# Kernel tuning notes

Measured on AMD Instinct MI355X. Metric: run time of the kernel, lower is better.

## Reference

```python
import jax, jax.numpy as jnp
import numpy as np

OUT_CH = 19  # out_channels


def setup_inputs() -> dict:
    key = jax.random.key(0)
    ks = jax.random.split(key, 8)
    N1, N2, C = 8000, 8000, 96
    return {
        "sur_sv_feature": jax.random.normal(ks[0], (N2, C), jnp.float32),
        "sur_sv_coords": jax.random.uniform(ks[1], (N2, 3), jnp.float32, -20.0, 20.0),
        "sur_sv_gt": jax.random.randint(ks[2], (N2,), 0, OUT_CH, dtype=jnp.int32),
        "sv_prob": jax.random.normal(ks[3], (N1, OUT_CH), jnp.float32),
        "mean_features": jax.random.normal(ks[4], (N1, C), jnp.float32),
        "ori_coords": jax.random.uniform(ks[5], (N1, 3), jnp.float32, -20.0, 20.0),
        # well-conditioned invertible 4x4 homogeneous poses
        "posses": jnp.eye(4, dtype=jnp.float32)[None, :, :] + 0.05 * jax.random.normal(ks[6], (2, 4, 4), jnp.float32),
        "sv_gt_idx": jax.random.randint(ks[7], (N2,), 0, N1, dtype=jnp.int32),  # unused in forward
        "lg": 8000,
    }


def _alignment(coords, posses):
    # rev=1 branch: diff = inv(poses[1]) @ poses[0]; aligned = (diff @ [coords,1]^T)^T[:, :3]
    diff = jnp.linalg.inv(posses[1]) @ posses[0]
    homo = jnp.concatenate([coords, jnp.ones((coords.shape[0], 1), coords.dtype)], axis=1)
    return (homo @ diff.T)[:, :3]


def reference(sur_sv_feature, sur_sv_coords, sur_sv_gt, sv_prob, mean_features, ori_coords, posses, sv_gt_idx, lg):
    N1 = sv_prob.shape[0]
    al = _alignment(sur_sv_coords, posses)  # [N2,3]
    # cosine distance [N1,N2]
    w1 = jnp.linalg.norm(mean_features, axis=1, keepdims=True)
    w2 = jnp.linalg.norm(sur_sv_feature, axis=1, keepdims=True)
    feat_dist_cos = 1.0 - (mean_features @ sur_sv_feature.T) / jnp.maximum(w1 * w2.T, 1e-8)
    # squared L2 distance [N1,N2], scaled by 1/0.5^2
    xn = jnp.sum(ori_coords ** 2, axis=1)[:, None]
    yn = jnp.sum(al ** 2, axis=1)[None, :]
    coords_dist = jnp.maximum(xn + yn - 2.0 * (ori_coords @ al.T), 0.0) / 0.25
    support = (coords_dist < 100.0).astype(jnp.float32)  # 10**2 radius gate
    onehot = jnp.eye(OUT_CH, dtype=jnp.float32)[sur_sv_gt]  # [N2,19]
    dist_matric = 1.0 + feat_dist_cos - jnp.exp(-0.5 * coords_dist)
    K = jnp.exp(-dist_matric / 0.03) * support
    # 'Sinkhorn' loop: b,a depend only on constants u1,u2, so each of the 10
    # iterations computes identical values -> compute once (bit-identical).
    u2 = jnp.full((K.shape[0],), 1.0 / K.shape[0], jnp.float32)
    u1 = jnp.full((K.shape[1],), 1.0 / K.shape[1], jnp.float32)
    b = u2 / (K @ u1 + 1e-16)      # [N1]
    a = u1 / (K.T @ u2 + 1e-16)    # [N2]
    # diag(a) @ K.T @ diag(b) = a[:,None] * K.T * b[None,:]  -> [N2,N1]
    sim = (a[:, None] * K.T) * b[None, :]
    sim = sim[:lg]
    sv_prob_updated = jax.nn.softmax(sv_prob, axis=1)
    sm_index = jnp.argmax(sim, axis=1)          # [lg] indices into N1
    tmpx = sur_sv_gt[:lg]                       # onehot[:lg].argmax == gt labels
    vals = sv_prob_updated[sm_index, tmpx]      # diag(P[sm_index].index_select(1,tmpx))
    mask = jnp.where(jnp.any(vals > 0.1), vals > 0.1, vals > 0.0)
    scatter_idx = jnp.where(mask, sm_index, N1)  # out-of-bounds sentinel -> dropped
    sv_prob_new = sv_prob_updated.at[scatter_idx].set(onehot[:lg], mode='drop')
    # torch.unique(sm_index[tmp]); padded with -1 for jit-static shape
    trust = jnp.unique(jnp.where(mask, sm_index, -1), size=lg, fill_value=-1)
    pre = jnp.argmax(sv_prob_new, axis=1)
    return (trust, mean_features, ori_coords, pre, sv_prob_new, trust)
```

## Files before the change

kernel.cpp:

```cpp
#include <hip/hip_runtime.h>

#define N 8000
#define C 96
#define C4 24
#define OCH 19
#define NCELL 1000
#define NCH 32
#define HSZ (NCH*NCELL)
#define U1 (1.0f/8000.0f)
#define PAIR_CAP 256

__device__ __forceinline__ int clamp10(int v) { return min(max(v, 0), 9); }

__global__ void __launch_bounds__(256) k_prep(
    const float* __restrict__ sf, const float* __restrict__ coords,
    const float* __restrict__ posses,
    float* __restrict__ w2, float4* __restrict__ alN,
    int* __restrict__ cellB, int* __restrict__ histB,
    int4* __restrict__ ck4, int4* __restrict__ wn4, int* __restrict__ flags) {
    int bx = blockIdx.x, tid = threadIdx.x;
    if (bx < 32) {
        __shared__ int lhist[NCELL];
        __shared__ float sdiff[12];
        for (int c = tid; c < NCELL; c += 256) lhist[c] = 0;
        int j = bx*256 + tid;
        if (tid == 0) {
            double M[4][8];
            for (int r = 0; r < 4; ++r)
                for (int c = 0; c < 4; ++c) {
                    M[r][c] = (double)posses[16 + r*4 + c];
                    M[r][4+c] = (r == c) ? 1.0 : 0.0;
                }
            for (int col = 0; col < 4; ++col) {
                int piv = col; double best = fabs(M[col][col]);
                for (int r = col+1; r < 4; ++r) { double v = fabs(M[r][col]); if (v > best) { best = v; piv = r; } }
                if (piv != col) for (int c = 0; c < 8; ++c) { double t = M[col][c]; M[col][c] = M[piv][c]; M[piv][c] = t; }
                double inv = 1.0 / M[col][col];
                for (int c = 0; c < 8; ++c) M[col][c] *= inv;
                for (int r = 0; r < 4; ++r) if (r != col) {
                    double f = M[r][col];
                    for (int c = 0; c < 8; ++c) M[r][c] -= f * M[col][c];
                }
            }
            for (int r = 0; r < 3; ++r)
                for (int c = 0; c < 4; ++c) {
                    double sm = 0.0;
                    for (int k = 0; k < 4; ++k) sm += M[r][4+k] * (double)posses[k*4 + c];
                    sdiff[r*4 + c] = (float)sm;
                }
        }
        __syncthreads();
        if (j < N) {
            float c0 = coords[j*3], c1 = coords[j*3+1], c2 = coords[j*3+2];
            float a0 = (sdiff[0]*c0 + sdiff[1]*c1) + (sdiff[2]*c2 + sdiff[3]);
            float a1 = (sdiff[4]*c0 + sdiff[5]*c1) + (sdiff[6]*c2 + sdiff[7]);
            float a2 = (sdiff[8]*c0 + sdiff[9]*c1) + (sdiff[10]*c2 + sdiff[11]);
            alN[j] = make_float4(a0, a1, a2, a0*a0 + a1*a1 + a2*a2);
            int cx = clamp10((int)floorf((a0 + 25.f) * 0.2f));
            int cy = clamp10((int)floorf((a1 + 25.f) * 0.2f));
            int cz = clamp10((int)floorf((a2 + 25.f) * 0.2f));
            int cc = (cz*10 + cy)*10 + cx;
            cellB[j] = cc;
            atomicAdd(&lhist[cc], 1);
        }
        __syncthreads();
        for (int c = tid; c < NCELL; c += 256) histB[bx*NCELL + c] = lhist[c];
    } else if (bx < 64) {
        int b = bx - 32;
        int u = tid & 3;
        #pragma unroll
        for (int p0 = 0; p0 < 256; p0 += 64) {
            int jp = b*256 + p0 + (tid >> 2);
            float ax = 0.f, ay = 0.f, az = 0.f, aw = 0.f;
            if (jp < N) {
                const float4* s4 = (const float4*)sf + jp*C4;
                #pragma unroll
                for (int s2 = 0; s2 < 6; ++s2) {
                    float4 v = s4[s2*4 + u];
                    ax += v.x*v.x; ay += v.y*v.y; az += v.z*v.z; aw += v.w*v.w;
                }
            }
            float pp = (ax + ay) + (az + aw);
            pp += __shfl_xor(pp, 1);
            pp += __shfl_xor(pp, 2);
            if (jp < N && u == 0) w2[jp] = sqrtf(pp);
        }
    } else {
        int t0 = (bx-64)*256 + tid;
        int4 z = make_int4(0, 0, 0, 0);
        int4 f = make_int4(-1, -1, -1, -1);
        for (int t = t0; t < 8000; t += 16*256) {
            if (t < 4000) ck4[t] = z;
            else wn4[t-4000] = f;
        }
        if (bx == 64 && tid < 8) flags[tid] = 0;
    }
}

__global__ void __launch_bounds__(1024) k_scan(int* __restrict__ h, int* __restrict__ cs) {
    int t = threadIdx.x;
    int v[NCH]; int tot = 0;
    if (t < NCELL) {
        #pragma unroll
        for (int ch = 0; ch < NCH; ++ch) { int x = h[ch*NCELL + t]; v[ch] = x; tot += x; }
    }
    int x = tot;
    int lane = t & 63, wv = t >> 6;
    for (int off = 1; off < 64; off <<= 1) { int y = __shfl_up(x, off); if (lane >= off) x += y; }
    __shared__ int wtot[16];
    if (lane == 63) wtot[wv] = x;
    __syncthreads();
    int wpre = 0;
    for (int k = 0; k < 16; ++k) if (k < wv) wpre += wtot[k];
    int base = wpre + x - tot;
    if (t < NCELL) {
        cs[t] = base;
        int run = base;
        #pragma unroll
        for (int ch = 0; ch < NCH; ++ch) { h[ch*NCELL + t] = run; run += v[ch]; }
    }
    if (t == 0) cs[NCELL] = N;
}

__global__ void k_scatter(const int* __restrict__ cellB, const int* __restrict__ startT,
                          const float* __restrict__ w2, const float4* __restrict__ alN,
                          int* __restrict__ idBR, float* __restrict__ w2R, float4* __restrict__ alR) {
    __shared__ int sc[256];
    int chunk = blockIdx.x, tid = threadIdx.x;
    int gi = chunk*256 + tid;
    int cell = (gi < N) ? cellB[gi] : -1;
    sc[tid] = cell;
    __syncthreads();
    if (gi >= N) return;
    int rank = 0;
    const int4* sc4 = (const int4*)sc;
    int full = tid >> 2;
    for (int t4 = 0; t4 < full; ++t4) {
        int4 q = sc4[t4];
        rank += (q.x == cell) + (q.y == cell) + (q.z == cell) + (q.w == cell);
    }
    for (int t = full*4; t < tid; ++t) rank += (sc[t] == cell);
    int pos = startT[chunk*NCELL + cell] + rank;
    idBR[pos] = gi;
    w2R[pos] = w2[gi];
    alR[pos] = alN[gi];
}

__global__ void __launch_bounds__(256) k_pairs(
    const float4* __restrict__ mf4, const float* __restrict__ ori,
    const float4* __restrict__ alR, const float* __restrict__ w2R,
    const float4* __restrict__ sf4, const int* __restrict__ idBR,
    const int* __restrict__ csB,
    unsigned long long* __restrict__ colkey) {
    __shared__ float4 sRow[4][C4];
    __shared__ int bgi[4][128];
    __shared__ float bc[4][128];
    __shared__ float bw[4][128];
    __shared__ int sJ[4][PAIR_CAP];
    __shared__ float sK[4][PAIR_CAP];

    int tid = threadIdx.x, lane = tid & 63, w = tid >> 6;
    int i = blockIdx.x * 4 + w;
    if (lane < C4) sRow[w][lane] = mf4[i*C4 + lane];
    __syncthreads();

    float ox = ori[i*3], oy = ori[i*3+1], oz = ori[i*3+2];
    float xnv = ox*ox + oy*oy + oz*oz;
    float s = 0.f;
    for (int kk = 0; kk < C4; ++kk) {
        float4 v = sRow[w][kk];
        s += v.x*v.x; s += v.y*v.y; s += v.z*v.z; s += v.w*v.w;
    }
    float w1v = sqrtf(s);

    int cx = clamp10((int)floorf((ox + 25.f) * 0.2f));
    int cy = clamp10((int)floorf((oy + 25.f) * 0.2f));
    int cz = clamp10((int)floorf((oz + 25.f) * 0.2f));
    int xlo = max(cx-1, 0), xhi = min(cx+1, 9);

    int s_[9], l_[9], c_[9];
    int tot = 0;
    #pragma unroll
    for (int t = 0; t < 9; ++t) {
        int z = cz + (t/3) - 1, y = cy + (t%3) - 1;
        bool ok = ((unsigned)z <= 9u) && ((unsigned)y <= 9u);
        int ss = 0, ee = 0;
        if (ok) {
            int cbase = (z*10 + y)*10;
            ss = csB[cbase + xlo];
            ee = csB[cbase + xhi + 1];
        }
        s_[t] = ss; l_[t] = ee - ss; c_[t] = tot; tot += ee - ss;
    }

    int cnt = 0, done = 0, npairs = 0;
    float racc = 0.f;
    unsigned long long lmask = (lane == 0) ? 0ull : (~0ull >> (64 - lane));
    int gu = lane & 3, gt_ = lane >> 2;

    auto process16 = [&](int nb) {
        int slot = (done + gt_) & 127;
        int gi = bgi[w][slot];
        float cdb = bc[w][slot];
        float w2v = bw[w][slot];
        float dotp = 0.f;
        if (gt_ < nb) {
            const float4* br = sf4 + gi*C4;
            float ax = 0.f, ay = 0.f, az = 0.f, aw = 0.f;
            #pragma unroll
            for (int s2 = 0; s2 < 6; ++s2) {
                int kk = s2*4 + gu;
                float4 a = sRow[w][kk];
                float4 b = br[kk];
                ax += a.x*b.x; ay += a.y*b.y; az += a.z*b.z; aw += a.w*b.w;
            }
            dotp = (ax + ay) + (az + aw);
        }
        dotp += __shfl_xor(dotp, 1);
        dotp += __shfl_xor(dotp, 2);
        if (gt_ < nb && gu == 0) {
            float fdc = 1.f - dotp / fmaxf(w1v * w2v, 1e-8f);
            float dist = (1.f + fdc) - expf(-0.5f * cdb);
            float K = expf(-dist / 0.03f);
            racc += K * U1;
            int sl = npairs + gt_;
            if (sl < PAIR_CAP) { sJ[w][sl] = gi; sK[w][sl] = K; }
        }
        npairs += nb;
        done += nb;
    };

    for (int f0 = 0; f0 < tot; f0 += 64) {
        int f = f0 + lane;
        bool act = f < tot;
        int q = 0;
        #pragma unroll
        for (int t = 0; t < 9; ++t) {
            bool in = (f >= c_[t]) && (f - c_[t] < l_[t]);
            if (in) q = s_[t] + (f - c_[t]);
        }
        bool pass = false; float cdv = 0.f;
        int jgi = 0; float jw2 = 0.f;
        if (act) {
            float4 aj = alR[q];
            jgi = idBR[q];
            jw2 = w2R[q];
            float d = xnv + aj.w - 2.f*(ox*aj.x + oy*aj.y + oz*aj.z);
            cdv = fmaxf(d, 0.f) * 4.f;
            pass = cdv < 100.f;
        }
        unsigned long long m = __ballot(pass);
        if (pass) {
            int slot = (cnt + __popcll(m & lmask)) & 127;
            bgi[w][slot] = jgi; bc[w][slot] = cdv; bw[w][slot] = jw2;
        }
        cnt += __popcll(m);
        if (cnt - done >= 64) {
            process16(16); process16(16); process16(16); process16(16);
        }
    }
    while (cnt > done) {
        int nb = cnt - done; if (nb > 16) nb = 16;
        process16(nb);
    }

    for (int off = 32; off; off >>= 1) racc += __shfl_xor(racc, off);
    float bi = U1 / (racc + 1e-16f);

    unsigned long long ikey = (unsigned long long)(unsigned)(N - i);
    int np = min(npairs, PAIR_CAP);
    for (int t = lane; t < np; t += 64) {
        float v = sK[w][t] * bi;
        if (v > 0.f) {
            unsigned long long key = ((unsigned long long)__float_as_uint(v) << 32) | ikey;
            atomicMax(&colkey[sJ[w][t]], key);
        }
    }
}

__global__ void k_post(const unsigned long long* __restrict__ colkey,
                       const float* __restrict__ sv_prob, const int* __restrict__ gt,
                       int* __restrict__ winnerHi, int* __restrict__ winnerLo,
                       int* __restrict__ flags) {
    int j = blockIdx.x * 256 + threadIdx.x;
    int lane = threadIdx.x & 63;
    bool valid = j < N;
    float vv = 0.f; int bidx = 0;
    if (valid) {
        unsigned long long key = colkey[j];
        bidx = key ? (N - (int)(key & 0xffffffffull)) : 0;
        const float* p = sv_prob + bidx*OCH;
        float m = -1e30f;
        for (int c = 0; c < OCH; ++c) m = fmaxf(m, p[c]);
        float ssum = 0.f, eg = 0.f; int g = gt[j];
        for (int c = 0; c < OCH; ++c) { float e = expf(p[c] - m); ssum += e; if (c == g) eg = e; }
        vv = eg / ssum;
    }
    bool hi = valid && (vv > 0.1f);
    bool nothi = valid && !(vv > 0.1f);
    bool lo = valid && (vv > 0.0f);
    bool notlo = valid && !(vv > 0.0f);
    if (hi) atomicMax(&winnerHi[bidx], j);
    if (lo) atomicMax(&winnerLo[bidx], j);
    unsigned long long m0 = __ballot(hi);
    unsigned long long m1 = __ballot(nothi);
    unsigned long long m2 = __ballot(notlo);
    if (lane == 0) {
        if (m0) atomicOr(&flags[0], 1);
        if (m1) atomicOr(&flags[1], 1);
        if (m2) atomicOr(&flags[2], 1);
    }
}

__global__ void __launch_bounds__(1024) k_final(
    const int* __restrict__ winnerHi, const int* __restrict__ winnerLo,
    const int* __restrict__ flags, const int* __restrict__ gt,
    const float* __restrict__ sv_prob,
    const float* __restrict__ mf, const float* __restrict__ ori,
    float* __restrict__ o_svp, float* __restrict__ o_pre,
    float* __restrict__ out0, float* __restrict__ out5,
    float* __restrict__ o_mf, float* __restrict__ o_ori) {
    int bx = blockIdx.x, tid = threadIdx.x;
    if (bx < 8) {
        const int* winner = flags[0] ? winnerHi : winnerLo;
        int i = bx*1024 + tid;
        if (i >= N) return;
        int w = winner[i];
        if (w >= 0) {
            int g = gt[w];
            for (int c = 0; c < OCH; ++c) o_svp[i*OCH + c] = (c == g) ? 1.f : 0.f;
            o_pre[i] = (float)g;
        } else {
            const float* p = sv_prob + i*OCH;
            float m = -1e30f;
            for (int c = 0; c < OCH; ++c) m = fmaxf(m, p[c]);
            float e[OCH]; float ssum = 0.f;
            for (int c = 0; c < OCH; ++c) { e[c] = expf(p[c] - m); ssum += e[c]; }
            float best = e[0] / ssum; int pidx = 0;
            o_svp[i*OCH] = best;
            for (int c = 1; c < OCH; ++c) {
                float r = e[c] / ssum;
                o_svp[i*OCH + c] = r;
                if (r > best) { best = r; pidx = c; }
            }
            o_pre[i] = (float)pidx;
        }
    } else if (bx == 8) {
        __shared__ int wsum[16];
        const int* winner = flags[0] ? winnerHi : winnerLo;
        int off = flags[0] ? (flags[1] ? 1 : 0) : (flags[2] ? 1 : 0);
        for (int p = tid; p < N; p += 1024) { out0[p] = -1.f; out5[p] = -1.f; }
        __syncthreads();
        int base = 0;
        for (int round = 0; round < N; round += 1024) {
            int i = round + tid;
            int pres = (i < N && winner[i] >= 0) ? 1 : 0;
            unsigned long long mask = __ballot(pres);
            int lane = tid & 63;
            int wv = tid >> 6;
            int excl = (lane == 0) ? 0 : __popcll(mask & (~0ull >> (64 - lane)));
            if (lane == 0) wsum[wv] = __popcll(mask);
            __syncthreads();
            int wpre = 0, tot = 0;
            for (int t = 0; t < 16; ++t) { if (t < wv) wpre += wsum[t]; tot += wsum[t]; }
            int pos = base + wpre + excl + off;
            if (pres && pos < N) { out0[pos] = (float)i; out5[pos] = (float)i; }
            base += tot;
            __syncthreads();
        }
    } else {
        const float4* mf4 = (const float4*)mf;
        const float4* ori4 = (const float4*)ori;
        float4* omf4 = (float4*)o_mf;
        float4* oori4 = (float4*)o_ori;
        int t0 = (bx-9)*1024 + tid;
        for (int t = t0; t < 198000; t += 51*1024) {
            if (t < 192000) omf4[t] = mf4[t];
            else oori4[t-192000] = ori4[t-192000];
        }
    }
}

extern "C" void kernel_launch(void* const* d_in, const int* in_sizes, int n_in,
                              void* d_out, int out_size, void* d_ws, size_t ws_size,
                              hipStream_t stream) {
    const float* sur_feat   = (const float*)d_in[0];
    const float* sur_coords = (const float*)d_in[1];
    const int*   sur_gt     = (const int*)d_in[2];
    const float* sv_prob    = (const float*)d_in[3];
    const float* mean_feat  = (const float*)d_in[4];
    const float* ori        = (const float*)d_in[5];
    const float* posses     = (const float*)d_in[6];

    float* out = (float*)d_out;
    float* o_trust  = out;
    float* o_mf     = out + 8000;
    float* o_ori    = out + 776000;
    float* o_pre    = out + 800000;
    float* o_svp    = out + 808000;
    float* o_trust2 = out + 960000;

    float* w = (float*)d_ws;
    float4* alN = (float4*)w;      w += 4*N;
    float4* alR = (float4*)w;      w += 4*N;
    unsigned long long* colkey = (unsigned long long*)w;  w += 4*N;
    float* w2 = w;                 w += N;
    float* w2R = w;                w += N;
    int* cellB = (int*)w;          w += N;
    int* histB = (int*)w;          w += HSZ;
    int* flags = (int*)w;          w += 8;
    int* csB = (int*)w;            w += 1008;
    int* idBR = (int*)w;           w += N;
    int* winnerHi = (int*)w;       w += N;
    int* winnerLo = (int*)w;       w += N;

    dim3 b256(256);

    k_prep<<<80, b256, 0, stream>>>(sur_feat, sur_coords, posses,
                                    w2, alN, cellB, histB,
                                    (int4*)colkey, (int4*)winnerHi, flags);
    k_scan<<<1, 1024, 0, stream>>>(histB, csB);
    k_scatter<<<32, b256, 0, stream>>>(cellB, histB, w2, alN, idBR, w2R, alR);
    k_pairs<<<N/4, b256, 0, stream>>>((const float4*)mean_feat, ori, alR, w2R,
                                      (const float4*)sur_feat, idBR, csB, colkey);
    k_post<<<32, b256, 0, stream>>>(colkey, sv_prob, sur_gt, winnerHi, winnerLo, flags);
    k_final<<<60, 1024, 0, stream>>>(winnerHi, winnerLo, flags, sur_gt, sv_prob,
                                     mean_feat, ori,
                                     o_svp, o_pre, o_trust, o_trust2, o_mf, o_ori);
}
```

Baseline: 67.84 us.

## Fold histogram scan into scatter kernel and prefetch next candidate batch in pairs

Result: no change. 66.70 us (-1.7%).

```diff
diff --git a/kernel.cpp b/kernel.cpp
--- a/kernel.cpp
+++ b/kernel.cpp
@@ -97,36 +97,44 @@
     }
 }
 
-__global__ void __launch_bounds__(1024) k_scan(int* __restrict__ h, int* __restrict__ cs) {
-    int t = threadIdx.x;
-    int v[NCH]; int tot = 0;
-    if (t < NCELL) {
-        #pragma unroll
-        for (int ch = 0; ch < NCH; ++ch) { int x = h[ch*NCELL + t]; v[ch] = x; tot += x; }
-    }
-    int x = tot;
-    int lane = t & 63, wv = t >> 6;
+__global__ void __launch_bounds__(256) k_scatter(
+    const int* __restrict__ cellB, const int* __restrict__ h,
+    const float* __restrict__ w2, const float4* __restrict__ alN,
+    int* __restrict__ idBR, float* __restrict__ w2R, float4* __restrict__ alR,
+    int* __restrict__ csB) {
+    __shared__ int sStart[NCELL];
+    __shared__ int wtot[4];
+    __shared__ int sc[256];
+    int chunk = blockIdx.x, tid = threadIdx.x;
+
+    int tot0 = 0, tot1 = 0, tot2 = 0, tot3 = 0;
+    int pre0 = 0, pre1 = 0, pre2 = 0, pre3 = 0;
+    bool cv = tid < 250;
+    if (cv) {
+        for (int ch = 0; ch < NCH; ++ch) {
+            int4 v = ((const int4*)(h + ch*NCELL))[tid];
+            tot0 += v.x; tot1 += v.y; tot2 += v.z; tot3 += v.w;
+            if (ch < chunk) { pre0 += v.x; pre1 += v.y; pre2 += v.z; pre3 += v.w; }
+        }
+    }
+    int S = tot0 + tot1 + tot2 + tot3;
+    int lane = tid & 63, wv = tid >> 6;
+    int x = S;
     for (int off = 1; off < 64; off <<= 1) { int y = __shfl_up(x, off); if (lane >= off) x += y; }
-    __shared__ int wtot[16];
     if (lane == 63) wtot[wv] = x;
     __syncthreads();
     int wpre = 0;
-    for (int k = 0; k < 16; ++k) if (k < wv) wpre += wtot[k];
-    int base = wpre + x - tot;
-    if (t < NCELL) {
-        cs[t] = base;
-        int run = base;
-        #pragma unroll
-        for (int ch = 0; ch < NCH; ++ch) { h[ch*NCELL + t] = run; run += v[ch]; }
-    }
-    if (t == 0) cs[NCELL] = N;
-}
-
-__global__ void k_scatter(const int* __restrict__ cellB, const int* __restrict__ startT,
-                          const float* __restrict__ w2, const float4* __restrict__ alN,
-                          int* __restrict__ idBR, float* __restrict__ w2R, float4* __restrict__ alR) {
-    __shared__ int sc[256];
-    int chunk = blockIdx.x, tid = threadIdx.x;
+    for (int k = 0; k < 4; ++k) if (k < wv) wpre += wtot[k];
+    int run = wpre + x - S;
+    if (cv) {
+        int c = tid*4;
+        sStart[c]   = run + pre0; if (chunk == 0) csB[c]   = run; run += tot0;
+        sStart[c+1] = run + pre1; if (chunk == 0) csB[c+1] = run; run += tot1;
+        sStart[c+2] = run + pre2; if (chunk == 0) csB[c+2] = run; run += tot2;
+        sStart[c+3] = run + pre3; if (chunk == 0) csB[c+3] = run; run += tot3;
+    }
+    if (chunk == 0 && tid == 0) csB[NCELL] = N;
+
     int gi = chunk*256 + tid;
     int cell = (gi < N) ? cellB[gi] : -1;
     sc[tid] = cell;
@@ -140,7 +148,7 @@
         rank += (q.x == cell) + (q.y == cell) + (q.z == cell) + (q.w == cell);
     }
     for (int t = full*4; t < tid; ++t) rank += (sc[t] == cell);
-    int pos = startT[chunk*NCELL + cell] + rank;
+    int pos = sStart[cell] + rank;
     idBR[pos] = gi;
     w2R[pos] = w2[gi];
     alR[pos] = alN[gi];
@@ -192,6 +200,16 @@
         }
         s_[t] = ss; l_[t] = ee - ss; c_[t] = tot; tot += ee - ss;
     }
+
+    auto calcq = [&](int f) -> int {
+        int q = 0;
+        #pragma unroll
+        for (int t = 0; t < 9; ++t) {
+            bool in = (f >= c_[t]) && (f - c_[t] < l_[t]);
+            if (in) q = s_[t] + (f - c_[t]);
+        }
+        return q;
+    };
 
     int cnt = 0, done = 0, npairs = 0;
     float racc = 0.f;
@@ -230,34 +248,38 @@
         done += nb;
     };
 
+    bool act_cur = lane < tot;
+    float4 aj_cur = make_float4(0.f, 0.f, 0.f, 0.f);
+    int gi_cur = 0; float w2_cur = 0.f;
+    if (act_cur) {
+        int q = calcq(lane);
+        aj_cur = alR[q]; gi_cur = idBR[q]; w2_cur = w2R[q];
+    }
     for (int f0 = 0; f0 < tot; f0 += 64) {
-        int f = f0 + lane;
-        bool act = f < tot;
-        int q = 0;
-        #pragma unroll
-        for (int t = 0; t < 9; ++t) {
-            bool in = (f >= c_[t]) && (f - c_[t] < l_[t]);
-            if (in) q = s_[t] + (f - c_[t]);
+        int fn = f0 + 64 + lane;
+        bool act_n = fn < tot;
+        float4 aj_n = make_float4(0.f, 0.f, 0.f, 0.f);
+        int gi_n = 0; float w2_n = 0.f;
+        if (act_n) {
+            int qn = calcq(fn);
+            aj_n = alR[qn]; gi_n = idBR[qn]; w2_n = w2R[qn];
         }
         bool pass = false; float cdv = 0.f;
-        int jgi = 0; float jw2 = 0.f;
-        if (act) {
-            float4 aj = alR[q];
-            jgi = idBR[q];
-            jw2 = w2R[q];
-            float d = xnv + aj.w - 2.f*(ox*aj.x + oy*aj.y + oz*aj.z);
+        if (act_cur) {
+            float d = xnv + aj_cur.w - 2.f*(ox*aj_cur.x + oy*aj_cur.y + oz*aj_cur.z);
             cdv = fmaxf(d, 0.f) * 4.f;
             pass = cdv < 100.f;
         }
         unsigned long long m = __ballot(pass);
         if (pass) {
             int slot = (cnt + __popcll(m & lmask)) & 127;
-            bgi[w][slot] = jgi; bc[w][slot] = cdv; bw[w][slot] = jw2;
+            bgi[w][slot] = gi_cur; bc[w][slot] = cdv; bw[w][slot] = w2_cur;
         }
         cnt += __popcll(m);
         if (cnt - done >= 64) {
             process16(16); process16(16); process16(16); process16(16);
         }
+        aj_cur = aj_n; gi_cur = gi_n; w2_cur = w2_n; act_cur = act_n;
     }
     while (cnt > done) {
         int nb = cnt - done; if (nb > 16) nb = 16;
@@ -419,8 +441,7 @@
     k_prep<<<80, b256, 0, stream>>>(sur_feat, sur_coords, posses,
                                     w2, alN, cellB, histB,
                                     (int4*)colkey, (int4*)winnerHi, flags);
-    k_scan<<<1, 1024, 0, stream>>>(histB, csB);
-    k_scatter<<<32, b256, 0, stream>>>(cellB, histB, w2, alN, idBR, w2R, alR);
+    k_scatter<<<32, b256, 0, stream>>>(cellB, histB, w2, alN, idBR, w2R, alR, csB);
     k_pairs<<<N/4, b256, 0, stream>>>((const float4*)mean_feat, ori, alR, w2R,
                                       (const float4*)sur_feat, idBR, csB, colkey);
     k_post<<<32, b256, 0, stream>>>(colkey, sv_prob, sur_gt, winnerHi, winnerLo, flags);
```
